# Optimization experiments

Hardware: AMD Instinct MI355X
Metric: run time of the kernel (lower is better)

The kernel has to match this reference:

```python
import jax, jax.numpy as jnp
import numpy as np

NUM_HEADS = 12
STEP_SIZE = 3

def softmax_1(a):
    # exp(a_i) / (1 + sum_j exp(a_j)), numerically stable
    m = jnp.maximum(jnp.max(a, axis=-1, keepdims=True), 0.0)
    e = jnp.exp(a - m)
    return e / (jnp.exp(-m) + jnp.sum(e, axis=-1, keepdims=True))

def setup_inputs() -> dict:
    key = jax.random.key(0)
    ks = jax.random.split(key, 7)
    B, N, C, L = 16, 4096, 768, 16
    s = C ** -0.5
    return {
        "x": jax.random.normal(ks[0], (B, N, C), dtype=jnp.float32),
        "query": jax.random.normal(ks[1], (1, L, C), dtype=jnp.float32),
        "Wq": jax.random.normal(ks[2], (C, C), dtype=jnp.float32) * s,
        "Wk": jax.random.normal(ks[3], (C, C), dtype=jnp.float32) * s,
        "Wv": jax.random.normal(ks[4], (C, C), dtype=jnp.float32) * s,
        "Wproj": jax.random.normal(ks[5], (C, C), dtype=jnp.float32) * s,
        "b_proj": jnp.zeros((C,), dtype=jnp.float32),
    }

def reference(x, query, Wq, Wk, Wv, Wproj, b_proj):
    B, N, C = x.shape
    H = NUM_HEADS
    hd = C // H
    L = query.shape[1]
    scale = hd ** -0.5
    # learned queries broadcast over batch
    queries = jnp.broadcast_to(query, (B, L, C))
    q = (queries @ Wq.T).reshape(B, L, H, hd).transpose(0, 2, 1, 3)  # [B,H,L,hd]
    k = (x @ Wk.T).reshape(B, N, H, hd).transpose(0, 2, 1, 3)        # [B,H,N,hd]
    v = k  # Hopfield update: state retrieves against stored patterns k
    for _ in range(STEP_SIZE):
        qs = q * scale
        attn = jnp.einsum('bhld,bhnd->bhln', qs, k)  # [B,H,L,N]
        attn = softmax_1(attn)
        q = jnp.einsum('bhln,bhnd->bhld', attn, v)   # [B,H,L,hd]
    out = q.transpose(0, 2, 1, 3).reshape(B, L, C)
    out = out @ Wv.T          # self.v output projection (no bias)
    out = out @ Wproj.T + b_proj  # self.proj
    return out
```

## Files before the change

### kernel.cpp

```cpp
#include <hip/hip_runtime.h>


typedef float  float4v  __attribute__((ext_vector_type(4)));
typedef short  short4v  __attribute__((ext_vector_type(4)));
typedef short  short8v  __attribute__((ext_vector_type(8)));
typedef unsigned int uint4v __attribute__((ext_vector_type(4)));
typedef short8v bf16x8;

__device__ __forceinline__ void splitbf(float v, unsigned int& hi, unsigned int& lo){
  unsigned int u = __float_as_uint(v);
  hi = u >> 16;
  float r = v - __uint_as_float(u & 0xffff0000u);
  lo = (__float_as_uint(r) + 0x8000u) >> 16;
}
__device__ __forceinline__ unsigned int packbf(float v){
  unsigned int u = __float_as_uint(v);
  float r = v - __uint_as_float(u & 0xffff0000u);
  return (u >> 16) | ((__float_as_uint(r) + 0x8000u) & 0xffff0000u);
}

__device__ __forceinline__ void gll16(const unsigned int* g, unsigned int* l){
  __builtin_amdgcn_global_load_lds(
      (const __attribute__((address_space(1))) unsigned int*)g,
      (__attribute__((address_space(3))) unsigned int*)l, 16, 0, 0);
}

__global__ __launch_bounds__(256)
void prep_kernel(const float* __restrict__ wk, unsigned short* __restrict__ dh,
                 unsigned short* __restrict__ dl,
                 const float* __restrict__ query, const float* __restrict__ wq,
                 float* __restrict__ q0){
  if(blockIdx.x < 576){
    size_t idx = (size_t)blockIdx.x*256 + threadIdx.x;
    float4v v = ((const float4v*)wk)[idx];
    short4v h4, l4;
    #pragma unroll
    for(int e=0;e<4;e++){
      unsigned int hh, ll;
      splitbf(v[e], hh, ll);
      h4[e] = (short)hh;
      l4[e] = (short)ll;
    }
    ((short4v*)dh)[idx] = h4;
    ((short4v*)dl)[idx] = l4;
  } else {
    int idx = (blockIdx.x - 576)*256 + threadIdx.x;
    int l = idx / 768, c = idx - l*768;
    const float* qr = query + l*768;
    const float* wr = wq + (size_t)c*768;
    float s = 0.f;
    for(int j=0;j<768;j+=4){
      float4v a  = *(const float4v*)(qr+j);
      float4v w4 = *(const float4v*)(wr+j);
      s += a[0]*w4[0]+a[1]*w4[1]+a[2]*w4[2]+a[3]*w4[3];
    }
    q0[idx] = s;
  }
}

__global__ __launch_bounds__(256, 3)
void gemm_k_kernel(const float* __restrict__ x, const unsigned short* __restrict__ wh,
                   const unsigned short* __restrict__ wl, unsigned int* __restrict__ khead){
  __shared__ unsigned short Ah[512*8], Al[512*8];
  const int tid  = threadIdx.x;
  const int id   = blockIdx.x;
  const int xcd  = id & 7, slot = id >> 3;
  const int bml  = slot / 6;
  const int bn   = slot - bml*6;
  const int bm   = xcd*64 + bml;
  const int wave = tid >> 6, lane = tid & 63, quad = lane >> 4, l16 = lane & 15;

  float4v acc[8][2];
  #pragma unroll
  for(int i=0;i<8;i++)
    #pragma unroll
    for(int j=0;j<2;j++) acc[i][j] = (float4v){0.f,0.f,0.f,0.f};

  const float* xA = x + (size_t)bm*128*768;
  const unsigned short* wbh = wh + (size_t)(bn*128 + wave*32 + l16)*768 + quad*8;
  const unsigned short* wbl = wl + (size_t)(bn*128 + wave*32 + l16)*768 + quad*8;

  const int row0 = tid >> 2, c8 = tid & 3;
  const int C0 = row0*4 + (c8 ^ ((row0 >> 2) & 3));
  const int C1 = C0 + 256;
  const float* g0 = xA + (size_t)row0*768 + c8*8;
  const float* g1 = g0 + (size_t)64*768;
  const int crd = l16*4 + (quad ^ ((l16 >> 2) & 3));

  float4v p00 = *(const float4v*)(g0);
  float4v p01 = *(const float4v*)(g0 + 4);
  float4v p10 = *(const float4v*)(g1);
  float4v p11 = *(const float4v*)(g1 + 4);

  for(int k0=0;k0<768;k0+=32){
    bf16x8 b_h[2], b_l[2];
    #pragma unroll
    for(int j=0;j<2;j++){
      b_h[j] = *(const bf16x8*)(wbh + (size_t)j*16*768 + k0);
      b_l[j] = *(const bf16x8*)(wbl + (size_t)j*16*768 + k0);
    }
    __syncthreads();

    {
      short8v hv, lv;
      #pragma unroll
      for(int e=0;e<4;e++){
        unsigned int hh, ll;
        splitbf(p00[e], hh, ll); hv[e]   = (short)hh; lv[e]   = (short)ll;
        splitbf(p01[e], hh, ll); hv[e+4] = (short)hh; lv[e+4] = (short)ll;
      }
      *(short8v*)(Ah + C0*8) = hv;
      *(short8v*)(Al + C0*8) = lv;
      #pragma unroll
      for(int e=0;e<4;e++){
        unsigned int hh, ll;
        splitbf(p10[e], hh, ll); hv[e]   = (short)hh; lv[e]   = (short)ll;
        splitbf(p11[e], hh, ll); hv[e+4] = (short)hh; lv[e+4] = (short)ll;
      }
      *(short8v*)(Ah + C1*8) = hv;
      *(short8v*)(Al + C1*8) = lv;
    }
    __syncthreads();

    if(k0 + 32 < 768){
      p00 = *(const float4v*)(g0 + k0 + 32);
      p01 = *(const float4v*)(g0 + k0 + 36);
      p10 = *(const float4v*)(g1 + k0 + 32);
      p11 = *(const float4v*)(g1 + k0 + 36);
    }

    #pragma unroll
    for(int i=0;i<8;i++){
      const unsigned short* ap = Ah + (size_t)(i*64 + crd)*8;
      const unsigned short* lp = Al + (size_t)(i*64 + crd)*8;
      bf16x8 a_h = *(const bf16x8*)ap;
      bf16x8 a_l = *(const bf16x8*)lp;
      #pragma unroll
      for(int j=0;j<2;j++){
        acc[i][j] = __builtin_amdgcn_mfma_f32_16x16x32_bf16(a_h, b_h[j], acc[i][j],0,0,0);
        acc[i][j] = __builtin_amdgcn_mfma_f32_16x16x32_bf16(a_l, b_h[j], acc[i][j],0,0,0);
        acc[i][j] = __builtin_amdgcn_mfma_f32_16x16x32_bf16(a_h, b_l[j], acc[i][j],0,0,0);
      }
    }
  }
  const int b     = bm >> 5;
  const int Cbase = bn*128 + wave*32;
  const int h     = Cbase >> 6;
  const int dbase = Cbase & 63;
  const int nn0   = (bm & 31)*128;
  unsigned int* kout = khead + (size_t)(b*12 + h)*262144;
  #pragma unroll
  for(int i=0;i<8;i++){
    #pragma unroll
    for(int r=0;r<4;r++){
      const int n   = nn0 + i*16 + quad*4 + r;
      const int row = n & 255, t = n >> 8;
      const int ph  = ((row & 7) << 2) ^ ((row & 8) << 1);
      unsigned int* kr = kout + (size_t)t*16384 + row*64;
      #pragma unroll
      for(int j=0;j<2;j++)
        kr[(dbase + j*16 + l16) ^ ph] = packbf(acc[i][j][r]);
    }
  }
}

__global__ __launch_bounds__(512, 2)
void attn3_kernel(const unsigned int* __restrict__ khead,
                  const float* __restrict__ q0g, float* __restrict__ qcur){
  __shared__ unsigned int knd[2*16384];
  float* accf  = (float*)(knd + 16384);
  float* lredf = (float*)(knd + 16384) + 8192;
  float* qtmp  = (float*)(knd + 16384) + 8320;

  const int tid  = threadIdx.x;
  const int bh   = blockIdx.x;
  const int b    = bh / 12;
  const int h    = bh - b*12;
  const int wave = tid >> 6, lane = tid & 63, quad = lane >> 4, l16 = lane & 15;

  const unsigned int* kg = khead + (size_t)bh*262144;
  const unsigned int* kwv = kg + wave*2048 + lane*4;
  unsigned int* lwv = knd + wave*2048;

  const int rowA = wave*32 + ((l16 >> 2) << 3) + (l16 & 3);
  const int rowB = rowA + 4;
  const int phiA = ((l16 & 3) << 2) ^ (((l16 >> 2) & 1) << 4);
  const int phiB = phiA ^ 16;
  const int q1   = quad & 1;

  #pragma unroll
  for(int g=0; g<8; ++g) gll16(kwv + g*256, lwv + g*256);

  for(int iter = 0; iter < 3; ++iter){
    const float* qrow = (iter == 0) ? (q0g + (size_t)l16*768 + h*64)
                                    : (qtmp + l16*64);
    bf16x8 qh[2], ql[2];
    #pragma unroll
    for(int s = 0; s < 2; ++s){
      float4v v0 = *(const float4v*)(qrow + s*32 + quad*8);
      float4v v1 = *(const float4v*)(qrow + s*32 + quad*8 + 4);
      #pragma unroll
      for(int e = 0; e < 8; ++e){
        float v = (e < 4 ? v0[e] : v1[e-4]) * 0.125f;
        unsigned int hh, ll;
        splitbf(v, hh, ll);
        qh[s][e] = (short)hh;
        ql[s][e] = (short)ll;
      }
    }
    __syncthreads();

    float4v acc[4];
    #pragma unroll
    for(int j=0;j<4;j++) acc[j] = (float4v){0.f,0.f,0.f,0.f};
    float lsum = 0.f;

    for(int t = 0; t < 16; ++t){
      const unsigned int* kcur = knd + ((t & 1) << 14);

      if(!(iter == 2 && t == 15)){
        const int tn = (t + 1) & 15;
        const unsigned int* gsrc = kwv + (size_t)tn*16384;
        unsigned int* ldst = lwv + (((t + 1) & 1) << 14);
        #pragma unroll
        for(int g=0; g<8; ++g) gll16(gsrc + g*256, ldst + g*256);
        asm volatile("s_waitcnt vmcnt(8)" ::: "memory");
      } else {
        asm volatile("s_waitcnt vmcnt(0)" ::: "memory");
      }
      __builtin_amdgcn_sched_barrier(0);

      float4v s1 = (float4v){0.f,0.f,0.f,0.f};
      float4v s2 = (float4v){0.f,0.f,0.f,0.f};
      #pragma unroll
      for(int s = 0; s < 2; ++s){
        const int c0 = s*32 + quad*8;
        uint4v w0 = *(const uint4v*)(kcur + rowA*64 + ((c0    ) ^ phiA));
        uint4v w1 = *(const uint4v*)(kcur + rowA*64 + ((c0 + 4) ^ phiA));
        uint4v u0 = *(const uint4v*)(kcur + rowB*64 + ((c0    ) ^ phiB));
        uint4v u1 = *(const uint4v*)(kcur + rowB*64 + ((c0 + 4) ^ phiB));
        bf16x8 a1h, a1l, a2h, a2l;
        #pragma unroll
        for(int j = 0; j < 4; ++j){
          a1h[j]   = (short)(w0[j] & 0xffffu);  a1l[j]   = (short)(w0[j] >> 16);
          a1h[j+4] = (short)(w1[j] & 0xffffu);  a1l[j+4] = (short)(w1[j] >> 16);
          a2h[j]   = (short)(u0[j] & 0xffffu);  a2l[j]   = (short)(u0[j] >> 16);
          a2h[j+4] = (short)(u1[j] & 0xffffu);  a2l[j+4] = (short)(u1[j] >> 16);
        }
        s1 = __builtin_amdgcn_mfma_f32_16x16x32_bf16(a1h, qh[s], s1, 0,0,0);
        s1 = __builtin_amdgcn_mfma_f32_16x16x32_bf16(a1l, qh[s], s1, 0,0,0);
        s1 = __builtin_amdgcn_mfma_f32_16x16x32_bf16(a1h, ql[s], s1, 0,0,0);
        s2 = __builtin_amdgcn_mfma_f32_16x16x32_bf16(a2h, qh[s], s2, 0,0,0);
        s2 = __builtin_amdgcn_mfma_f32_16x16x32_bf16(a2l, qh[s], s2, 0,0,0);
        s2 = __builtin_amdgcn_mfma_f32_16x16x32_bf16(a2h, ql[s], s2, 0,0,0);
      }

      bf16x8 pa_h, pa_l;
      #pragma unroll
      for(int e = 0; e < 4; ++e){
        float v = __expf(s1[e]);
        lsum += v;
        unsigned int hh, ll;
        splitbf(v, hh, ll);
        pa_h[e] = (short)hh;
        pa_l[e] = (short)ll;
        float v2 = __expf(s2[e]);
        lsum += v2;
        splitbf(v2, hh, ll);
        pa_h[e+4] = (short)hh;
        pa_l[e+4] = (short)ll;
      }

      const int rb0 = wave*32 + quad*8;
      #pragma unroll
      for(int j = 0; j < 4; ++j){
        bf16x8 kbh, kbl;
        #pragma unroll
        for(int e = 0; e < 8; ++e){
          const int jx = ((e >> 2) ^ q1) & 1;
          unsigned int w = kcur[(rb0 + e)*64 + ((j ^ jx) << 4) + (l16 ^ ((e & 3) << 2))];
          kbh[e] = (short)(w & 0xffffu);
          kbl[e] = (short)(w >> 16);
        }
        acc[j] = __builtin_amdgcn_mfma_f32_16x16x32_bf16(pa_h, kbh, acc[j], 0,0,0);
        acc[j] = __builtin_amdgcn_mfma_f32_16x16x32_bf16(pa_l, kbh, acc[j], 0,0,0);
        acc[j] = __builtin_amdgcn_mfma_f32_16x16x32_bf16(pa_h, kbl, acc[j], 0,0,0);
      }
    }

    __syncthreads();
    lsum += __shfl_xor(lsum, 16);
    lsum += __shfl_xor(lsum, 32);
    if(quad == 0) lredf[wave*16 + l16] = lsum;
    #pragma unroll
    for(int j = 0; j < 4; ++j)
      #pragma unroll
      for(int r = 0; r < 4; ++r)
        accf[wave*1024 + (quad*4 + r)*64 + j*16 + l16] = acc[j][r];
    __syncthreads();
    #pragma unroll
    for(int k = 0; k < 2; ++k){
      const int i = tid + k*512;
      const int l = i >> 6, d = i & 63;
      float s = 0.f, lt = 1.f;
      #pragma unroll
      for(int w = 0; w < 8; ++w){ s += accf[w*1024 + i]; }
      #pragma unroll
      for(int w = 0; w < 8; ++w){ lt += lredf[w*16 + l]; }
      const float qv = s / lt;
      if(iter < 2) qtmp[i] = qv;
      else qcur[(size_t)(b*16 + l)*768 + h*64 + d] = qv;
    }
    __syncthreads();
  }
}

__global__ __launch_bounds__(256)
void proj_kernel(const float* __restrict__ inp, const float* __restrict__ w,
                 const float* __restrict__ bias, float* __restrict__ out){
  __shared__ float rows[4*768];
  const int r0 = blockIdx.x*4;
  const int c  = blockIdx.y*256 + threadIdx.x;
  for(int j = threadIdx.x; j < 4*768; j += 256) rows[j] = inp[(size_t)r0*768 + j];
  __syncthreads();
  const float* wr = w + (size_t)c*768;
  float a0=0.f, a1=0.f, a2=0.f, a3=0.f;
  for(int j=0;j<768;j+=4){
    float4v w4 = *(const float4v*)(wr+j);
    float4v r0v = *(const float4v*)(rows+j);
    float4v r1v = *(const float4v*)(rows+768+j);
    float4v r2v = *(const float4v*)(rows+1536+j);
    float4v r3v = *(const float4v*)(rows+2304+j);
    #pragma unroll
    for(int e=0;e<4;e++){
      a0 += r0v[e]*w4[e]; a1 += r1v[e]*w4[e];
      a2 += r2v[e]*w4[e]; a3 += r3v[e]*w4[e];
    }
  }
  const float bb = bias ? bias[c] : 0.f;
  out[(size_t)(r0+0)*768 + c] = a0 + bb;
  out[(size_t)(r0+1)*768 + c] = a1 + bb;
  out[(size_t)(r0+2)*768 + c] = a2 + bb;
  out[(size_t)(r0+3)*768 + c] = a3 + bb;
}

extern "C" void kernel_launch(void* const* d_in, const int* in_sizes, int n_in,
                              void* d_out, int out_size, void* d_ws, size_t ws_size,
                              hipStream_t stream){
  const float* x     = (const float*)d_in[0];
  const float* query = (const float*)d_in[1];
  const float* Wq    = (const float*)d_in[2];
  const float* Wk    = (const float*)d_in[3];
  const float* Wv    = (const float*)d_in[4];
  const float* Wproj = (const float*)d_in[5];
  const float* bproj = (const float*)d_in[6];
  float* out = (float*)d_out;

  char* ws = (char*)d_ws;
  unsigned int*   khead = (unsigned int*)(ws);
  float*          qcur  = (float*)(ws + 201326592);
  float*          q0    = (float*)(ws + 202113024);
  char*           R     = ws + 202162176;
  unsigned short* wkh   = (unsigned short*)(R);
  unsigned short* wkl   = (unsigned short*)(R + 1179648);
  float*          out1  = (float*)(R);

  prep_kernel<<<624, 256, 0, stream>>>(Wk, wkh, wkl, query, Wq, q0);
  gemm_k_kernel<<<3072, 256, 0, stream>>>(x, wkh, wkl, khead);

  attn3_kernel<<<192, 512, 0, stream>>>(khead, q0, qcur);

  proj_kernel<<<dim3(64, 3), 256, 0, stream>>>(qcur, Wv, nullptr, out1);
  proj_kernel<<<dim3(64, 3), 256, 0, stream>>>(out1, Wproj, bproj, out);
}
```

Before: 661.6 us.

## Fuse first Hopfield iteration into K-projection GEMM epilogue with atomic reduction

The GEMM epilogue now stages each 128-row K tile in shared memory. It computes unnormalised exp(q0·k) scores for the two heads that tile covers and accumulates partial exp-weighted K sums and exp sums into global buffers with atomicAdd. Those buffers are zeroed by extra blocks in the prep kernel. The attention kernel then forms the first-iteration query by dividing by 1 plus the sum, and runs only the remaining two iterations. This removes one full pass over the 4096 keys per head in the low-parallelism attention kernel. The cost is scalar FP32 work, extra LDS and atomics in the GEMM, and dropping the max subtraction in the first softmax, which relies on the scores staying small.

```diff
diff --git a/kernel.cpp b/kernel.cpp
--- a/kernel.cpp
+++ b/kernel.cpp
@@ -29,9 +29,11 @@
 void prep_kernel(const float* __restrict__ wk, unsigned short* __restrict__ dh,
                  unsigned short* __restrict__ dl,
                  const float* __restrict__ query, const float* __restrict__ wq,
-                 float* __restrict__ q0){
-  if(blockIdx.x < 576){
-    size_t idx = (size_t)blockIdx.x*256 + threadIdx.x;
+                 float* __restrict__ q0,
+                 float* __restrict__ pacc, float* __restrict__ plsum){
+  const int bid = blockIdx.x;
+  if(bid < 576){
+    size_t idx = (size_t)bid*256 + threadIdx.x;
     float4v v = ((const float4v*)wk)[idx];
     short4v h4, l4;
     #pragma unroll
@@ -43,8 +45,8 @@
     }
     ((short4v*)dh)[idx] = h4;
     ((short4v*)dl)[idx] = l4;
-  } else {
-    int idx = (blockIdx.x - 576)*256 + threadIdx.x;
+  } else if(bid < 624){
+    int idx = (bid - 576)*256 + threadIdx.x;
     int l = idx / 768, c = idx - l*768;
     const float* qr = query + l*768;
     const float* wr = wq + (size_t)c*768;
@@ -55,13 +57,22 @@
       s += a[0]*w4[0]+a[1]*w4[1]+a[2]*w4[2]+a[3]*w4[3];
     }
     q0[idx] = s;
+  } else if(bid < 1392){
+    pacc[(size_t)(bid - 624)*256 + threadIdx.x] = 0.f;
+  } else {
+    plsum[(bid - 1392)*256 + threadIdx.x] = 0.f;
   }
 }
 
 __global__ __launch_bounds__(256, 3)
 void gemm_k_kernel(const float* __restrict__ x, const unsigned short* __restrict__ wh,
-                   const unsigned short* __restrict__ wl, unsigned int* __restrict__ khead){
+                   const unsigned short* __restrict__ wl, unsigned int* __restrict__ khead,
+                   const float* __restrict__ q0g,
+                   float* __restrict__ pacc, float* __restrict__ plsum){
   __shared__ unsigned short Ah[512*8], Al[512*8];
+  __shared__ float kt[32*128];
+  __shared__ float q0s[2*16*64];
+  __shared__ float ep[32*16*2];
   const int tid  = threadIdx.x;
   const int id   = blockIdx.x;
   const int xcd  = id & 7, slot = id >> 3;
@@ -100,7 +111,6 @@
       b_l[j] = *(const bf16x8*)(wbl + (size_t)j*16*768 + k0);
     }
     __syncthreads();
-
     {
       short8v hv, lv;
       #pragma unroll
@@ -131,10 +141,8 @@
 
     #pragma unroll
     for(int i=0;i<8;i++){
-      const unsigned short* ap = Ah + (size_t)(i*64 + crd)*8;
-      const unsigned short* lp = Al + (size_t)(i*64 + crd)*8;
-      bf16x8 a_h = *(const bf16x8*)ap;
-      bf16x8 a_l = *(const bf16x8*)lp;
+      bf16x8 a_h = *(const bf16x8*)(Ah + (size_t)(i*64 + crd)*8);
+      bf16x8 a_l = *(const bf16x8*)(Al + (size_t)(i*64 + crd)*8);
       #pragma unroll
       for(int j=0;j<2;j++){
         acc[i][j] = __builtin_amdgcn_mfma_f32_16x16x32_bf16(a_h, b_h[j], acc[i][j],0,0,0);
@@ -143,6 +151,7 @@
       }
     }
   }
+
   const int b     = bm >> 5;
   const int Cbase = bn*128 + wave*32;
   const int h     = Cbase >> 6;
@@ -162,11 +171,73 @@
         kr[(dbase + j*16 + l16) ^ ph] = packbf(acc[i][j][r]);
     }
   }
+
+  {
+    const int h0 = bn*2;
+    for(int idx = tid; idx < 2048; idx += 256){
+      const int hp = idx >> 10, l = (idx >> 6) & 15, d = idx & 63;
+      q0s[idx] = q0g[l*768 + (h0 + hp)*64 + d] * 0.125f;
+    }
+    const int ho = tid >> 7, lo = (tid >> 3) & 15, d8 = tid & 7;
+    float pr[8];
+    #pragma unroll
+    for(int e=0;e<8;e++) pr[e] = 0.f;
+    float pl = 0.f;
+    for(int g = 0; g < 4; ++g){
+      __syncthreads();
+      #pragma unroll
+      for(int ii = 0; ii < 2; ++ii){
+        const int i = g*2 + ii;
+        #pragma unroll
+        for(int j = 0; j < 2; ++j)
+          #pragma unroll
+          for(int r = 0; r < 4; ++r)
+            kt[(ii*16 + quad*4 + r)*128 + wave*32 + j*16 + l16] = acc[i][j][r];
+      }
+      __syncthreads();
+      {
+        const int n = tid & 31, lb = (tid >> 5) << 1;
+        #pragma unroll
+        for(int dl = 0; dl < 2; ++dl)
+          #pragma unroll
+          for(int hp = 0; hp < 2; ++hp){
+            float s = 0.f;
+            const float* qp = q0s + hp*1024 + (lb + dl)*64;
+            const float* kp = kt + n*128 + hp*64;
+            #pragma unroll
+            for(int d = 0; d < 64; d += 4){
+              float4v a  = *(const float4v*)(qp + d);
+              float4v kk = *(const float4v*)(kp + d);
+              s += a[0]*kk[0] + a[1]*kk[1] + a[2]*kk[2] + a[3]*kk[3];
+            }
+            ep[(n*16 + lb + dl)*2 + hp] = __expf(s);
+          }
+      }
+      __syncthreads();
+      {
+        const float* kb = kt + ho*64 + d8*8;
+        #pragma unroll
+        for(int n = 0; n < 32; ++n){
+          const float e = ep[(n*16 + lo)*2 + ho];
+          pl += e;
+          const float4v k0 = *(const float4v*)(kb + n*128);
+          const float4v k1 = *(const float4v*)(kb + n*128 + 4);
+          pr[0] += e*k0[0]; pr[1] += e*k0[1]; pr[2] += e*k0[2]; pr[3] += e*k0[3];
+          pr[4] += e*k1[0]; pr[5] += e*k1[1]; pr[6] += e*k1[2]; pr[7] += e*k1[3];
+        }
+      }
+    }
+    float* pa = pacc + (size_t)(b*12 + h0 + ho)*1024 + lo*64 + d8*8;
+    #pragma unroll
+    for(int e=0;e<8;e++) atomicAdd(pa + e, pr[e]);
+    if(d8 == 0) atomicAdd(plsum + (b*12 + h0 + ho)*16 + lo, pl);
+  }
 }
 
 __global__ __launch_bounds__(512, 2)
 void attn3_kernel(const unsigned int* __restrict__ khead,
-                  const float* __restrict__ q0g, float* __restrict__ qcur){
+                  const float* __restrict__ pacc, const float* __restrict__ plsum,
+                  float* __restrict__ qcur){
   __shared__ unsigned int knd[2*16384];
   float* accf  = (float*)(knd + 16384);
   float* lredf = (float*)(knd + 16384) + 8192;
@@ -191,9 +262,15 @@
   #pragma unroll
   for(int g=0; g<8; ++g) gll16(kwv + g*256, lwv + g*256);
 
-  for(int iter = 0; iter < 3; ++iter){
-    const float* qrow = (iter == 0) ? (q0g + (size_t)l16*768 + h*64)
-                                    : (qtmp + l16*64);
+  #pragma unroll
+  for(int k2 = 0; k2 < 2; ++k2){
+    const int i = tid + k2*512;
+    qtmp[i] = pacc[(size_t)bh*1024 + i] / (1.f + plsum[bh*16 + (i >> 6)]);
+  }
+  __syncthreads();
+
+  for(int iter = 1; iter < 3; ++iter){
+    const float* qrow = qtmp + l16*64;
     bf16x8 qh[2], ql[2];
     #pragma unroll
     for(int s = 0; s < 2; ++s){
@@ -358,17 +435,18 @@
 
   char* ws = (char*)d_ws;
   unsigned int*   khead = (unsigned int*)(ws);
-  float*          qcur  = (float*)(ws + 201326592);
-  float*          q0    = (float*)(ws + 202113024);
-  char*           R     = ws + 202162176;
-  unsigned short* wkh   = (unsigned short*)(R);
-  unsigned short* wkl   = (unsigned short*)(R + 1179648);
-  float*          out1  = (float*)(R);
-
-  prep_kernel<<<624, 256, 0, stream>>>(Wk, wkh, wkl, query, Wq, q0);
-  gemm_k_kernel<<<3072, 256, 0, stream>>>(x, wkh, wkl, khead);
-
-  attn3_kernel<<<192, 512, 0, stream>>>(khead, q0, qcur);
+  float*          plsum = (float*)(ws + 201326592);
+  float*          q0    = (float*)(ws + 201338880);
+  unsigned short* wkh   = (unsigned short*)(ws + 201388032);
+  unsigned short* wkl   = (unsigned short*)(ws + 202567680);
+  float*          qcur  = (float*)(ws + 201388032);
+  float*          out1  = (float*)(ws + 202567680);
+  float*          pacc  = (float*)d_out;
+
+  prep_kernel<<<1404, 256, 0, stream>>>(Wk, wkh, wkl, query, Wq, q0, pacc, plsum);
+  gemm_k_kernel<<<3072, 256, 0, stream>>>(x, wkh, wkl, khead, q0, pacc, plsum);
+
+  attn3_kernel<<<192, 512, 0, stream>>>(khead, pacc, plsum, qcur);
 
   proj_kernel<<<dim3(64, 3), 256, 0, stream>>>(qcur, Wv, nullptr, out1);
   proj_kernel<<<dim3(64, 3), 256, 0, stream>>>(out1, Wproj, bproj, out);
```

Result: slower. 1.583 ms (+139.2%).
